# Kernel optimization log

Measured on AMD Instinct MI355X. Metric: run time of the kernel, lower is better.

## Reference

```python
import jax, jax.numpy as jnp
import numpy as np

D_MODEL, N_HEADS, D_K, D_V = 1024, 16, 64, 64


def setup_inputs() -> dict:
    key = jax.random.key(0)
    ks = jax.random.split(key, 9)
    B, S = 8, 1024
    Q = jax.random.normal(ks[0], (B, S, D_MODEL), dtype=jnp.float32)
    K = jax.random.normal(ks[1], (B, S, D_MODEL), dtype=jnp.float32)
    V = jax.random.normal(ks[2], (B, S, D_MODEL), dtype=jnp.float32)
    # Xavier-uniform weights (gain=1): limit = sqrt(6/(fan_in+fan_out))
    lim = float(np.sqrt(6.0 / (D_MODEL + N_HEADS * D_K)))
    Wq = jax.random.uniform(ks[3], (D_MODEL, N_HEADS * D_K), minval=-lim, maxval=lim, dtype=jnp.float32)
    Wk = jax.random.uniform(ks[4], (D_MODEL, N_HEADS * D_K), minval=-lim, maxval=lim, dtype=jnp.float32)
    Wv = jax.random.uniform(ks[5], (D_MODEL, N_HEADS * D_V), minval=-lim, maxval=lim, dtype=jnp.float32)
    # nn.Linear default bias init: uniform(-1/sqrt(fan_in), 1/sqrt(fan_in))
    bl = float(1.0 / np.sqrt(D_MODEL))
    bq = jax.random.uniform(ks[6], (N_HEADS * D_K,), minval=-bl, maxval=bl, dtype=jnp.float32)
    bk = jax.random.uniform(ks[7], (N_HEADS * D_K,), minval=-bl, maxval=bl, dtype=jnp.float32)
    bv = jax.random.uniform(ks[8], (N_HEADS * D_V,), minval=-bl, maxval=bl, dtype=jnp.float32)
    return {"Q": Q, "K": K, "V": V, "Wq": Wq, "bq": bq, "Wk": Wk, "bk": bk, "Wv": Wv, "bv": bv}


def reference(Q, K, V, Wq, bq, Wk, bk, Wv, bv):
    B, S, _ = Q.shape
    # projections -> [B, H, S, d]
    q = (Q @ Wq + bq).reshape(B, S, N_HEADS, D_K).transpose(0, 2, 1, 3)
    k = (K @ Wk + bk).reshape(B, S, N_HEADS, D_K).transpose(0, 2, 1, 3)
    v = (V @ Wv + bv).reshape(B, S, N_HEADS, D_V).transpose(0, 2, 1, 3)
    scores = jnp.exp(jnp.einsum('bhqd,bhkd->bhqk', q, k) / jnp.sqrt(jnp.float32(D_K)))
    attn = scores / (jnp.sum(scores, axis=-1, keepdims=True) + 1e-8)
    ctx = jnp.einsum('bhqk,bhkd->bhqd', attn, v)  # [B,H,S,Dv]
    return ctx.transpose(0, 2, 1, 3).reshape(B, S, N_HEADS * D_V)
```

## Files before the change

### kernel.cpp

```cpp
#include <hip/hip_runtime.h>
#include <stdint.h>

#define DM 1024
#define HEADS 16
#define BATCH 8
#define SEQ 1024
#define MTOT 8192

typedef _Float16 half8 __attribute__((ext_vector_type(8)));
typedef _Float16 half4 __attribute__((ext_vector_type(4)));
typedef float floatx4 __attribute__((ext_vector_type(4)));

__device__ __forceinline__ void glds16(const void* g, void* l) {
    __builtin_amdgcn_global_load_lds(
        (const __attribute__((address_space(1))) void*)g,
        (__attribute__((address_space(3))) void*)l, 16, 0, 0);
}

__global__ __launch_bounds__(256) void prep(
        const float* __restrict__ Q, const float* __restrict__ K,
        const float* __restrict__ V,
        _Float16* __restrict__ qb, _Float16* __restrict__ kb, _Float16* __restrict__ vb,
        const float* __restrict__ Wq, const float* __restrict__ Wk,
        const float* __restrict__ Wv,
        _Float16* __restrict__ wqt, _Float16* __restrict__ wkt, _Float16* __restrict__ wvt) {
    __shared__ float t[32][33];
    int bid = blockIdx.x, tid = threadIdx.x;
    if (bid < 12288) {
        int ten = bid >> 12;
        int bx  = bid & 4095;
        const float* src = ten == 0 ? Q : (ten == 1 ? K : V);
        _Float16* dst    = ten == 0 ? qb : (ten == 1 ? kb : vb);
        size_t i = ((size_t)bx * 256 + tid) * 8;
        float4 a = *(const float4*)(src + i);
        float4 b = *(const float4*)(src + i + 4);
        half8 h;
        h[0] = (_Float16)a.x; h[1] = (_Float16)a.y; h[2] = (_Float16)a.z; h[3] = (_Float16)a.w;
        h[4] = (_Float16)b.x; h[5] = (_Float16)b.y; h[6] = (_Float16)b.z; h[7] = (_Float16)b.w;
        *(half8*)(dst + i) = h;
    } else {
        int wb = bid - 12288;
        int z  = wb >> 10;
        int rem = wb & 1023;
        const float* W = z == 0 ? Wq : (z == 1 ? Wk : Wv);
        _Float16* Wt   = z == 0 ? wqt : (z == 1 ? wkt : wvt);
        int k0 = (rem & 31) * 32, n0 = (rem >> 5) * 32;
        int tx = tid & 31, ty = tid >> 5;
#pragma unroll
        for (int i = 0; i < 4; i++)
            t[ty + i * 8][tx] = W[(size_t)(k0 + ty + i * 8) * DM + n0 + tx];
        __syncthreads();
#pragma unroll
        for (int i = 0; i < 4; i++)
            Wt[(size_t)(n0 + ty + i * 8) * DM + k0 + tx] = (_Float16)t[tx][ty + i * 8];
    }
}

__global__ __launch_bounds__(256) void proj_gemm(
        const _Float16* __restrict__ qb, const _Float16* __restrict__ kb,
        const _Float16* __restrict__ vb,
        const _Float16* __restrict__ wqt, const _Float16* __restrict__ wkt,
        const _Float16* __restrict__ wvt,
        const float* __restrict__ bq, const float* __restrict__ bk,
        const float* __restrict__ bv,
        _Float16* __restrict__ qh, _Float16* __restrict__ kh, _Float16* __restrict__ vT) {
    __shared__ _Float16 As[128 * 64];
    __shared__ _Float16 Bs[128 * 64];
    int z = blockIdx.z;
    const _Float16* A  = z == 0 ? qb : (z == 1 ? kb : vb);
    const _Float16* Bw = z == 0 ? wqt : (z == 1 ? wkt : wvt);
    const float* bias  = z == 0 ? bq : (z == 1 ? bk : bv);
    int m0 = blockIdx.x * 128, n0 = blockIdx.y * 128;
    int tid = threadIdx.x, wid = tid >> 6, lane = tid & 63;
    int l15 = lane & 15, quad = lane >> 4;
    int wm = wid >> 1, wn = wid & 1;
    bool swapped = (z < 2);

    floatx4 acc[4][4] = {};

    for (int kb_ = 0; kb_ < 16; kb_++) {
        __syncthreads();
        int k0 = kb_ * 64;
        int r = (wid * 4) * 8 + (lane >> 3);
        int pg = (lane & 7) ^ (lane >> 3);
#pragma unroll
        for (int ii = 0; ii < 4; ii++) {
            int issue = wid * 4 + ii;
            int rr = r + ii * 8;
            glds16(A  + (size_t)(m0 + rr) * DM + k0 + pg * 8, &As[issue * 512]);
            glds16(Bw + (size_t)(n0 + rr) * DM + k0 + pg * 8, &Bs[issue * 512]);
        }
        __syncthreads();
#pragma unroll
        for (int kc = 0; kc < 2; kc++) {
            half8 a[4], b[4];
#pragma unroll
            for (int mt = 0; mt < 4; mt++) {
                int row = wm * 64 + mt * 16 + l15;
                int pl = (kc * 4 + quad) ^ (l15 & 7);
                a[mt] = *(const half8*)&As[row * 64 + pl * 8];
            }
#pragma unroll
            for (int nt = 0; nt < 4; nt++) {
                int row = wn * 64 + nt * 16 + l15;
                int pl = (kc * 4 + quad) ^ (l15 & 7);
                b[nt] = *(const half8*)&Bs[row * 64 + pl * 8];
            }
            if (swapped) {
#pragma unroll
                for (int mt = 0; mt < 4; mt++)
#pragma unroll
                    for (int nt = 0; nt < 4; nt++)
                        acc[mt][nt] = __builtin_amdgcn_mfma_f32_16x16x32_f16(
                            b[nt], a[mt], acc[mt][nt], 0, 0, 0);
            } else {
#pragma unroll
                for (int mt = 0; mt < 4; mt++)
#pragma unroll
                    for (int nt = 0; nt < 4; nt++)
                        acc[mt][nt] = __builtin_amdgcn_mfma_f32_16x16x32_f16(
                            a[mt], b[nt], acc[mt][nt], 0, 0, 0);
            }
        }
    }

    if (swapped) {
        float sc = (z == 0) ? 0.125f : 1.0f;
        _Float16* out = (z == 0) ? qh : kh;
#pragma unroll
        for (int nt = 0; nt < 4; nt++) {
            int d0 = n0 + wn * 64 + nt * 16 + quad * 4;
            int hh = d0 >> 6, dd = d0 & 63;
            floatx4 b4 = *(const floatx4*)&bias[d0];
#pragma unroll
            for (int mt = 0; mt < 4; mt++) {
                int s = m0 + wm * 64 + mt * 16 + l15;
                int b_ = s >> 10, ss = s & 1023;
                size_t off = ((size_t)(b_ * HEADS + hh)) * 65536 + (size_t)ss * 64 + dd;
                half4 hv;
#pragma unroll
                for (int r = 0; r < 4; r++)
                    hv[r] = (_Float16)((acc[mt][nt][r] + b4[r]) * sc);
                *(half4*)&out[off] = hv;
            }
        }
    } else {
#pragma unroll
        for (int nt = 0; nt < 4; nt++) {
            int d = n0 + wn * 64 + nt * 16 + l15;
            int hh = d >> 6, dd = d & 63;
            float bv_ = bias[d];
#pragma unroll
            for (int mt = 0; mt < 4; mt++) {
                int s0 = m0 + wm * 64 + mt * 16 + quad * 4;
                int b_ = s0 >> 10, ss = s0 & 1023;
                size_t off = ((size_t)(b_ * HEADS + hh)) * 65536 + (size_t)dd * 1024 + ss;
                half4 hv;
#pragma unroll
                for (int r = 0; r < 4; r++)
                    hv[r] = (_Float16)(acc[mt][nt][r] + bv_);
                *(half4*)&vT[off] = hv;
            }
        }
    }
}

__global__ __launch_bounds__(256) void attn(
        const _Float16* __restrict__ qh, const _Float16* __restrict__ kh,
        const _Float16* __restrict__ vT, float* __restrict__ out) {
    __shared__ _Float16 Ks[4096];
    __shared__ _Float16 Vs[4096];
    __shared__ _Float16 QP[16384];
    int qt = blockIdx.x, h = blockIdx.y, b = blockIdx.z;
    size_t base = ((size_t)(b * HEADS + h)) * 65536;
    int tid = threadIdx.x, wid = tid >> 6, lane = tid & 63;
    int l15 = lane & 15, quad = lane >> 4;
    int rs = lane >> 3;
    int pg = (lane & 7) ^ rs;

#pragma unroll
    for (int ii = 0; ii < 8; ii++) {
        int issue = wid * 8 + ii;
        int r = issue * 8 + rs;
        glds16(qh + base + (size_t)(qt * 256 + r) * 64 + pg * 8, &QP[issue * 512]);
    }
    __syncthreads();
    half8 qf[4][2];
#pragma unroll
    for (int mt = 0; mt < 4; mt++)
#pragma unroll
        for (int kc = 0; kc < 2; kc++) {
            int row = wid * 64 + mt * 16 + l15;
            int pl = (kc * 4 + quad) ^ (l15 & 7);
            qf[mt][kc] = *(const half8*)&QP[row * 64 + pl * 8];
        }
    __syncthreads();

    floatx4 oacc[4][4] = {};
    float rden[4] = {0.f, 0.f, 0.f, 0.f};
    _Float16* Pw = &QP[wid * 4096];

    for (int kt = 0; kt < 16; kt++) {
        __syncthreads();
#pragma unroll
        for (int ii = 0; ii < 2; ii++) {
            int issue = wid * 2 + ii;
            int r = issue * 8 + rs;
            glds16(kh + base + (size_t)(kt * 64 + r) * 64 + pg * 8, &Ks[issue * 512]);
            glds16(vT + base + (size_t)r * 1024 + kt * 64 + pg * 8, &Vs[issue * 512]);
        }
        __syncthreads();

#pragma unroll
        for (int hf = 0; hf < 2; hf++) {
            floatx4 sacc[2][4] = {};
#pragma unroll
            for (int kc = 0; kc < 2; kc++) {
                half8 kf[2];
#pragma unroll
                for (int kn2 = 0; kn2 < 2; kn2++) {
                    int kn = hf * 2 + kn2;
                    int pl = (kc * 4 + quad) ^ (l15 & 7);
                    kf[kn2] = *(const half8*)&Ks[(kn * 16 + l15) * 64 + pl * 8];
                }
#pragma unroll
                for (int kn2 = 0; kn2 < 2; kn2++)
#pragma unroll
                    for (int mt = 0; mt < 4; mt++)
                        sacc[kn2][mt] = __builtin_amdgcn_mfma_f32_16x16x32_f16(
                            kf[kn2], qf[mt][kc], sacc[kn2][mt], 0, 0, 0);
            }
#pragma unroll
            for (int kn2 = 0; kn2 < 2; kn2++) {
                int kn = hf * 2 + kn2;
#pragma unroll
                for (int mt = 0; mt < 4; mt++) {
                    half4 ph;
#pragma unroll
                    for (int r = 0; r < 4; r++) {
                        float p = __expf(sacc[kn2][mt][r]);
                        rden[mt] += p;
                        ph[r] = (_Float16)p;
                    }
                    *(half4*)&Pw[(kn * 2 + (quad >> 1)) * 512 + (mt * 16 + l15) * 8 +
                                 (quad & 1) * 4] = ph;
                }
            }
            half8 af[4], vf[4];
#pragma unroll
            for (int mt = 0; mt < 4; mt++)
                af[mt] = *(const half8*)&Pw[(hf * 4 + quad) * 512 + (mt * 16 + l15) * 8];
#pragma unroll
            for (int dn = 0; dn < 4; dn++) {
                int pl = (hf * 4 + quad) ^ (l15 & 7);
                vf[dn] = *(const half8*)&Vs[(dn * 16 + l15) * 64 + pl * 8];
            }
#pragma unroll
            for (int mt = 0; mt < 4; mt++)
#pragma unroll
                for (int dn = 0; dn < 4; dn++)
                    oacc[mt][dn] = __builtin_amdgcn_mfma_f32_16x16x32_f16(
                        af[mt], vf[dn], oacc[mt][dn], 0, 0, 0);
        }
    }

#pragma unroll
    for (int mt = 0; mt < 4; mt++) {
        float d = rden[mt];
        d += __shfl_xor(d, 16, 64);
        d += __shfl_xor(d, 32, 64);
        rden[mt] = 1.0f / (d + 1e-8f);
    }
#pragma unroll
    for (int mt = 0; mt < 4; mt++) {
#pragma unroll
        for (int r = 0; r < 4; r++) {
            float dinv = __shfl(rden[mt], quad * 4 + r, 16);
            int s = qt * 256 + wid * 64 + mt * 16 + quad * 4 + r;
#pragma unroll
            for (int dn = 0; dn < 4; dn++) {
                int col = h * 64 + dn * 16 + l15;
                out[((size_t)(b * SEQ + s)) * 1024 + col] = oacc[mt][dn][r] * dinv;
            }
        }
    }
}

extern "C" void kernel_launch(void* const* d_in, const int* in_sizes, int n_in,
                              void* d_out, int out_size, void* d_ws, size_t ws_size,
                              hipStream_t stream) {
    const float* Q  = (const float*)d_in[0];
    const float* K  = (const float*)d_in[1];
    const float* V  = (const float*)d_in[2];
    const float* Wq = (const float*)d_in[3];
    const float* bq = (const float*)d_in[4];
    const float* Wk = (const float*)d_in[5];
    const float* bk = (const float*)d_in[6];
    const float* Wv = (const float*)d_in[7];
    const float* bv = (const float*)d_in[8];
    float* out = (float*)d_out;

    char* ws = (char*)d_ws;
    const size_t TEN = (size_t)MTOT * DM * sizeof(_Float16);
    _Float16* qb  = (_Float16*)(ws);
    _Float16* kb  = (_Float16*)(ws + TEN);
    _Float16* vb  = (_Float16*)(ws + 2 * TEN);
    _Float16* qh  = (_Float16*)(ws + 3 * TEN);
    _Float16* kh  = (_Float16*)(ws + 4 * TEN);
    _Float16* vT  = (_Float16*)(ws + 5 * TEN);
    const size_t WTN = (size_t)DM * DM * sizeof(_Float16);
    _Float16* wqt = (_Float16*)(ws + 6 * TEN);
    _Float16* wkt = (_Float16*)(ws + 6 * TEN + WTN);
    _Float16* wvt = (_Float16*)(ws + 6 * TEN + 2 * WTN);

    prep<<<dim3(15360), 256, 0, stream>>>(Q, K, V, qb, kb, vb,
                                          Wq, Wk, Wv, wqt, wkt, wvt);
    proj_gemm<<<dim3(64, 8, 3), 256, 0, stream>>>(qb, kb, vb, wqt, wkt, wvt,
                                                  bq, bk, bv, qh, kh, vT);
    attn<<<dim3(4, 16, 8), 256, 0, stream>>>(qh, kh, vT, out);
}
```

Baseline: 277.1 us.

## Enlarge projection GEMM tiles to 256x256 with double-buffered LDS prefetch

The projection GEMM moves from 128x128 tiles with 4 waves to 256x256 tiles with 8 waves, each wave computing a 128x64 sub-tile. The K loop now double-buffers LDS and issues the next tile's global-to-LDS loads in two halves interleaved with the MFMA work, with one barrier per iteration instead of two. This aims to raise arithmetic intensity and hide load latency. The costs are 128KB of LDS per block, more accumulator registers, and only 384 blocks, which may leave CUs underused or lower occupancy.

```diff
diff --git a/kernel.cpp b/kernel.cpp
--- a/kernel.cpp
+++ b/kernel.cpp
@@ -56,7 +56,7 @@
     }
 }
 
-__global__ __launch_bounds__(256) void proj_gemm(
+__global__ __launch_bounds__(512, 2) void proj_gemm(
         const _Float16* __restrict__ qb, const _Float16* __restrict__ kb,
         const _Float16* __restrict__ vb,
         const _Float16* __restrict__ wqt, const _Float16* __restrict__ wkt,
@@ -64,64 +64,124 @@
         const float* __restrict__ bq, const float* __restrict__ bk,
         const float* __restrict__ bv,
         _Float16* __restrict__ qh, _Float16* __restrict__ kh, _Float16* __restrict__ vT) {
-    __shared__ _Float16 As[128 * 64];
-    __shared__ _Float16 Bs[128 * 64];
+    __shared__ _Float16 lds[65536];
+    _Float16* As = lds;
+    _Float16* Bs = lds + 32768;
     int z = blockIdx.z;
     const _Float16* A  = z == 0 ? qb : (z == 1 ? kb : vb);
     const _Float16* Bw = z == 0 ? wqt : (z == 1 ? wkt : wvt);
     const float* bias  = z == 0 ? bq : (z == 1 ? bk : bv);
-    int m0 = blockIdx.x * 128, n0 = blockIdx.y * 128;
+    int m0 = blockIdx.x * 256, n0 = blockIdx.y * 256;
     int tid = threadIdx.x, wid = tid >> 6, lane = tid & 63;
     int l15 = lane & 15, quad = lane >> 4;
-    int wm = wid >> 1, wn = wid & 1;
+    int wm = wid >> 2, wn = wid & 3;
     bool swapped = (z < 2);
 
-    floatx4 acc[4][4] = {};
-
-    for (int kb_ = 0; kb_ < 16; kb_++) {
-        __syncthreads();
-        int k0 = kb_ * 64;
-        int r = (wid * 4) * 8 + (lane >> 3);
-        int pg = (lane & 7) ^ (lane >> 3);
-#pragma unroll
-        for (int ii = 0; ii < 4; ii++) {
-            int issue = wid * 4 + ii;
-            int rr = r + ii * 8;
-            glds16(A  + (size_t)(m0 + rr) * DM + k0 + pg * 8, &As[issue * 512]);
-            glds16(Bw + (size_t)(n0 + rr) * DM + k0 + pg * 8, &Bs[issue * 512]);
-        }
-        __syncthreads();
-#pragma unroll
-        for (int kc = 0; kc < 2; kc++) {
-            half8 a[4], b[4];
-#pragma unroll
-            for (int mt = 0; mt < 4; mt++) {
-                int row = wm * 64 + mt * 16 + l15;
-                int pl = (kc * 4 + quad) ^ (l15 & 7);
-                a[mt] = *(const half8*)&As[row * 64 + pl * 8];
-            }
-#pragma unroll
-            for (int nt = 0; nt < 4; nt++) {
+    int srow = lane >> 3;
+    int pg = (lane & 7) ^ srow;
+
+    floatx4 acc[8][4] = {};
+
+#pragma unroll
+    for (int r = 0; r < 4; r++) {
+        int rowA = r * 64 + wid * 8;
+        glds16(A  + (size_t)(m0 + rowA + srow) * DM + pg * 8, &As[rowA * 64]);
+        glds16(Bw + (size_t)(n0 + rowA + srow) * DM + pg * 8, &Bs[rowA * 64]);
+    }
+    __syncthreads();
+
+    for (int t = 0; t < 16; t++) {
+        int buf  = (t & 1) << 14;
+        int nbuf = buf ^ 16384;
+        int kn0 = (t + 1) * 64;
+
+        if (t < 15) {
+#pragma unroll
+            for (int r = 0; r < 2; r++) {
+                int rowA = r * 64 + wid * 8;
+                glds16(A  + (size_t)(m0 + rowA + srow) * DM + kn0 + pg * 8,
+                       &As[nbuf + rowA * 64]);
+                glds16(Bw + (size_t)(n0 + rowA + srow) * DM + kn0 + pg * 8,
+                       &Bs[nbuf + rowA * 64]);
+            }
+        }
+        half8 bfr[4][2];
+#pragma unroll
+        for (int nt = 0; nt < 4; nt++)
+#pragma unroll
+            for (int kc = 0; kc < 2; kc++) {
                 int row = wn * 64 + nt * 16 + l15;
                 int pl = (kc * 4 + quad) ^ (l15 & 7);
-                b[nt] = *(const half8*)&Bs[row * 64 + pl * 8];
-            }
-            if (swapped) {
+                bfr[nt][kc] = *(const half8*)&Bs[buf + row * 64 + pl * 8];
+            }
+        half8 afr[4][2];
+#pragma unroll
+        for (int mt = 0; mt < 4; mt++)
+#pragma unroll
+            for (int kc = 0; kc < 2; kc++) {
+                int row = wm * 128 + mt * 16 + l15;
+                int pl = (kc * 4 + quad) ^ (l15 & 7);
+                afr[mt][kc] = *(const half8*)&As[buf + row * 64 + pl * 8];
+            }
+        if (swapped) {
+#pragma unroll
+            for (int kc = 0; kc < 2; kc++)
 #pragma unroll
                 for (int mt = 0; mt < 4; mt++)
 #pragma unroll
                     for (int nt = 0; nt < 4; nt++)
                         acc[mt][nt] = __builtin_amdgcn_mfma_f32_16x16x32_f16(
-                            b[nt], a[mt], acc[mt][nt], 0, 0, 0);
-            } else {
+                            bfr[nt][kc], afr[mt][kc], acc[mt][nt], 0, 0, 0);
+        } else {
+#pragma unroll
+            for (int kc = 0; kc < 2; kc++)
 #pragma unroll
                 for (int mt = 0; mt < 4; mt++)
 #pragma unroll
                     for (int nt = 0; nt < 4; nt++)
                         acc[mt][nt] = __builtin_amdgcn_mfma_f32_16x16x32_f16(
-                            a[mt], b[nt], acc[mt][nt], 0, 0, 0);
-            }
-        }
+                            afr[mt][kc], bfr[nt][kc], acc[mt][nt], 0, 0, 0);
+        }
+
+        if (t < 15) {
+#pragma unroll
+            for (int r = 2; r < 4; r++) {
+                int rowA = r * 64 + wid * 8;
+                glds16(A  + (size_t)(m0 + rowA + srow) * DM + kn0 + pg * 8,
+                       &As[nbuf + rowA * 64]);
+                glds16(Bw + (size_t)(n0 + rowA + srow) * DM + kn0 + pg * 8,
+                       &Bs[nbuf + rowA * 64]);
+            }
+        }
+#pragma unroll
+        for (int mt = 0; mt < 4; mt++)
+#pragma unroll
+            for (int kc = 0; kc < 2; kc++) {
+                int row = wm * 128 + 64 + mt * 16 + l15;
+                int pl = (kc * 4 + quad) ^ (l15 & 7);
+                afr[mt][kc] = *(const half8*)&As[buf + row * 64 + pl * 8];
+            }
+        if (swapped) {
+#pragma unroll
+            for (int kc = 0; kc < 2; kc++)
+#pragma unroll
+                for (int mt = 0; mt < 4; mt++)
+#pragma unroll
+                    for (int nt = 0; nt < 4; nt++)
+                        acc[4 + mt][nt] = __builtin_amdgcn_mfma_f32_16x16x32_f16(
+                            bfr[nt][kc], afr[mt][kc], acc[4 + mt][nt], 0, 0, 0);
+        } else {
+#pragma unroll
+            for (int kc = 0; kc < 2; kc++)
+#pragma unroll
+                for (int mt = 0; mt < 4; mt++)
+#pragma unroll
+                    for (int nt = 0; nt < 4; nt++)
+                        acc[4 + mt][nt] = __builtin_amdgcn_mfma_f32_16x16x32_f16(
+                            afr[mt][kc], bfr[nt][kc], acc[4 + mt][nt], 0, 0, 0);
+        }
+
+        __syncthreads();
     }
 
     if (swapped) {
@@ -133,8 +193,8 @@
             int hh = d0 >> 6, dd = d0 & 63;
             floatx4 b4 = *(const floatx4*)&bias[d0];
 #pragma unroll
-            for (int mt = 0; mt < 4; mt++) {
-                int s = m0 + wm * 64 + mt * 16 + l15;
+            for (int mt = 0; mt < 8; mt++) {
+                int s = m0 + wm * 128 + mt * 16 + l15;
                 int b_ = s >> 10, ss = s & 1023;
                 size_t off = ((size_t)(b_ * HEADS + hh)) * 65536 + (size_t)ss * 64 + dd;
                 half4 hv;
@@ -151,8 +211,8 @@
             int hh = d >> 6, dd = d & 63;
             float bv_ = bias[d];
 #pragma unroll
-            for (int mt = 0; mt < 4; mt++) {
-                int s0 = m0 + wm * 64 + mt * 16 + quad * 4;
+            for (int mt = 0; mt < 8; mt++) {
+                int s0 = m0 + wm * 128 + mt * 16 + quad * 4;
                 int b_ = s0 >> 10, ss = s0 & 1023;
                 size_t off = ((size_t)(b_ * HEADS + hh)) * 65536 + (size_t)dd * 1024 + ss;
                 half4 hv;
@@ -315,7 +375,7 @@
 
     prep<<<dim3(15360), 256, 0, stream>>>(Q, K, V, qb, kb, vb,
                                           Wq, Wk, Wv, wqt, wkt, wvt);
-    proj_gemm<<<dim3(64, 8, 3), 256, 0, stream>>>(qb, kb, vb, wqt, wkt, wvt,
+    proj_gemm<<<dim3(32, 4, 3), 512, 0, stream>>>(qb, kb, vb, wqt, wkt, wvt,
                                                   bq, bk, bv, qh, kh, vT);
     attn<<<dim3(4, 16, 8), 256, 0, stream>>>(qh, kh, vT, out);
 }
```

Result: slower. 408.2 us (+47.3%).
